# Optimization experiments

Hardware: AMD Instinct MI355X
Metric: run time of the kernel (lower is better)

## Reference

```python
import jax, jax.numpy as jnp
import numpy as np

EMB = 1024
NHEAD = 16
DILATIONS = (1, 4, 8, 16)
KSIZE = 7
ROT_DIM = 32  # RotaryEmbedding(dim=32): only first 32 channels of each head rotated


def neighbor_idx(T, k, d):
    # NATTEN-style 1D dilated neighborhood: window of k positions on the
    # dilation lattice (same residue class mod d), centered and clamped at borders.
    i = jnp.arange(T)
    r = i % d                      # residue class
    p = i // d                     # position within class
    Lr = (T - r + d - 1) // d      # class length
    s = jnp.clip(p - k // 2, 0, Lr - k)
    j = jnp.arange(k)
    return r[:, None] + (s[:, None] + j[None, :]) * d  # [T, k] int indices


def rope(x, rot_dim=ROT_DIM):
    # lucidrains RotaryEmbedding.rotate_queries_or_keys: interleaved pairs,
    # applied over seq dim (-2), only first rot_dim channels.
    T = x.shape[-2]
    inv = 1.0 / (10000.0 ** (jnp.arange(0, rot_dim, 2, dtype=jnp.float32) / rot_dim))
    freqs = jnp.arange(T, dtype=jnp.float32)[:, None] * inv[None, :]  # [T, rot_dim//2]
    freqs = jnp.repeat(freqs, 2, axis=-1)                             # [T, rot_dim]
    cos, sin = jnp.cos(freqs), jnp.sin(freqs)
    xr, xp = x[..., :rot_dim], x[..., rot_dim:]
    x1, x2 = xr[..., 0::2], xr[..., 1::2]
    rot = jnp.stack([-x2, x1], axis=-1).reshape(xr.shape)
    return jnp.concatenate([xr * cos + rot * sin, xp], axis=-1)


def setup_inputs() -> dict:
    key = jax.random.key(0)
    ks = jax.random.split(key, 5)
    B, T, C = 4, 8192, EMB
    s = 0.02
    return {
        "x": jax.random.normal(ks[0], (B, T, C), jnp.float32),
        "wq": jax.random.normal(ks[1], (C, C), jnp.float32) * s,
        "bq": jnp.zeros((C,), jnp.float32),
        "wk": jax.random.normal(ks[2], (C, C), jnp.float32) * s,
        "bk": jnp.zeros((C,), jnp.float32),
        "wv": jax.random.normal(ks[3], (C, C), jnp.float32) * s,
        "bv": jnp.zeros((C,), jnp.float32),
        "wp": jax.random.normal(ks[4], (C, C), jnp.float32) * s,
        "bp": jnp.zeros((C,), jnp.float32),
    }


def reference(x, wq, bq, wk, bk, wv, bv, wp, bp):
    B, T, C = x.shape
    hs = C // NHEAD

    def heads(w, b):  # torch Linear: x @ W^T + b, then [B, nh, T, hs]
        return (x @ w.T + b).reshape(B, T, NHEAD, hs).transpose(0, 2, 1, 3)

    q, k, v = heads(wq, bq), heads(wk, bk), heads(wv, bv)
    present = jnp.stack([k, v])  # pre-rotary kv cache, as in original

    q, k, v = rope(q), rope(k), rope(v)  # original also rotates v

    gsz = NHEAD // len(DILATIONS)
    outs = []
    for gi, d in enumerate(DILATIONS):
        sl = slice(gi * gsz, (gi + 1) * gsz)
        idx = neighbor_idx(T, KSIZE, d)           # [T, K]
        kk = k[:, sl][:, :, idx]                   # [B, g, T, K, hs]
        vv = v[:, sl][:, :, idx]                   # [B, g, T, K, hs]
        scores = jnp.einsum('bgtd,bgtkd->bgtk', q[:, sl], kk)  # no 1/sqrt(hs), as na1d_qk
        attn = jax.nn.softmax(scores, axis=-1)
        outs.append(jnp.einsum('bgtk,bgtkd->bgtd', attn, vv))
    y = jnp.concatenate(outs, axis=1)              # [B, nh, T, hs]
    y = y.transpose(0, 2, 1, 3).reshape(B, T, C)
    y = y @ wp.T + bp
    return (y, present)
```

## Files before the change

kernel.cpp:

```cpp
#include <hip/hip_runtime.h>

typedef unsigned short ushortT;
typedef unsigned int uint32;
typedef __attribute__((ext_vector_type(8))) short short8;
typedef __attribute__((ext_vector_type(4))) float f32x4;

__device__ __forceinline__ ushortT f2bf(float f) {
    uint32 u = __float_as_uint(f);
    uint32 r = (u + 0x7fffu + ((u >> 16) & 1u)) >> 16;
    return (ushortT)r;
}
__device__ __forceinline__ float bf2f(uint32 v) {
    return __uint_as_float(v << 16);
}

__device__ __forceinline__ void unpack8(uint4 v, float* f) {
    f[0] = bf2f(v.x & 0xffffu); f[1] = bf2f(v.x >> 16);
    f[2] = bf2f(v.y & 0xffffu); f[3] = bf2f(v.y >> 16);
    f[4] = bf2f(v.z & 0xffffu); f[5] = bf2f(v.z >> 16);
    f[6] = bf2f(v.w & 0xffffu); f[7] = bf2f(v.w >> 16);
}

typedef __attribute__((address_space(1))) const void gvoid;
typedef __attribute__((address_space(3))) void lvoid;
__device__ __forceinline__ void gld16(const ushortT* g, ushortT* l) {
    __builtin_amdgcn_global_load_lds((gvoid*)g, (lvoid*)l, 16, 0, 0);
}

__global__ __launch_bounds__(256) void f32_to_bf16_kernel(
    const float* __restrict__ src, ushortT* __restrict__ dst, int n4)
{
    int i = blockIdx.x * 256 + threadIdx.x;
    if (i < n4) {
        float4 v = reinterpret_cast<const float4*>(src)[i];
        ushort4 o;
        o.x = f2bf(v.x); o.y = f2bf(v.y); o.z = f2bf(v.z); o.w = f2bf(v.w);
        reinterpret_cast<ushort4*>(dst)[i] = o;
    }
}

__global__ __launch_bounds__(256) void rope_table_kernel(float2* __restrict__ tab)
{
    int idx = blockIdx.x * 256 + threadIdx.x;
    int t = idx >> 4;
    int i = idx & 15;
    float inv = powf(10000.0f, -(float)i / 16.0f);
    float ang = (float)t * inv;
    tab[idx] = make_float2(cosf(ang), sinf(ang));
}


__device__ __forceinline__ short8 ldsfrag(const ushortT* region, int row, int g) {
    int e = (row << 5) + (g << 3);
    e ^= ((row >> 1) & 3) << 3;
    return *reinterpret_cast<const short8*>(region + e);
}

template<int MODE>
__global__ __launch_bounds__(512, 2) void gemm256_kernel(
    const ushortT* __restrict__ A,
    const ushortT* __restrict__ W,
    const float*   __restrict__ bias,
    const float2*  __restrict__ tab,
    ushortT*       __restrict__ Cb,
    float*         __restrict__ Cf,
    int M, int N, int K)
{
    extern __shared__ ushortT lds[];
    const int tid  = threadIdx.x;
    const int lane = tid & 63;
    const int wv   = tid >> 6;
    const int wm   = wv >> 2;
    const int wn   = wv & 3;
    const int g    = lane >> 4;
    const int rsel = lane & 15;

    const int bid = blockIdx.x;
    const int swz = (bid & 7) * 64 + (bid >> 3);
    const int tm  = swz & 127, tn = swz >> 7;
    const int m0  = tm * 256,  n0 = tn * 256;

    const int crow = tid >> 2;
    const int ccol = ((tid & 3) ^ ((tid >> 3) & 3)) * 8;
    const ushortT* gA0 = A + (size_t)(m0 + crow) * K + ccol;
    const ushortT* gA1 = gA0 + (size_t)128 * K;
    const ushortT* gB0 = W + (size_t)(n0 + crow) * K + ccol;
    const ushortT* gB1 = gB0 + (size_t)128 * K;

    const int dst0 = wv * 512;
    const int dst1 = 4096 + wv * 512;

    #pragma unroll
    for (int t = 0; t < 3; ++t) {
        ushortT* ra = lds + t * 16384;
        ushortT* rb = ra + 8192;
        gld16(gA0 + t * 32, ra + dst0);
        gld16(gA1 + t * 32, ra + dst1);
        gld16(gB0 + t * 32, rb + dst0);
        gld16(gB1 + t * 32, rb + dst1);
    }
    asm volatile("s_waitcnt vmcnt(8)" ::: "memory");
    __builtin_amdgcn_s_barrier();

    f32x4 acc[8][4] = {};
    const int NT = K >> 5;

    #pragma unroll 1
    for (int t = 0; t < NT; ++t) {
        const ushortT* ra = lds + (t & 3) * 16384;
        const ushortT* rb = ra + 8192;

        short8 Bf[4], Af[4];
        #pragma unroll
        for (int fn = 0; fn < 4; ++fn) Bf[fn] = ldsfrag(rb, wn * 64 + fn * 16 + rsel, g);
        #pragma unroll
        for (int fm = 0; fm < 4; ++fm) Af[fm] = ldsfrag(ra, wm * 128 + fm * 16 + rsel, g);
        if (t + 3 < NT) {
            ushortT* wa = lds + ((t + 3) & 3) * 16384;
            gld16(gA0 + (t + 3) * 32, wa + dst0);
            gld16(gA1 + (t + 3) * 32, wa + dst1);
        }
        asm volatile("" ::: "memory");
        __builtin_amdgcn_s_barrier();
        asm volatile("s_waitcnt lgkmcnt(0)" ::: "memory");
        __builtin_amdgcn_sched_barrier(0);
        __builtin_amdgcn_s_setprio(1);
        #pragma unroll
        for (int fm = 0; fm < 4; ++fm)
            #pragma unroll
            for (int fn = 0; fn < 4; ++fn)
                acc[fm][fn] = __builtin_amdgcn_mfma_f32_16x16x32_bf16(Af[fm], Bf[fn], acc[fm][fn], 0, 0, 0);
        __builtin_amdgcn_s_setprio(0);
        asm volatile("" ::: "memory");
        __builtin_amdgcn_s_barrier();

        #pragma unroll
        for (int fm = 0; fm < 4; ++fm) Af[fm] = ldsfrag(ra, wm * 128 + 64 + fm * 16 + rsel, g);
        if (t + 3 < NT) {
            ushortT* wb = lds + ((t + 3) & 3) * 16384 + 8192;
            gld16(gB0 + (t + 3) * 32, wb + dst0);
            gld16(gB1 + (t + 3) * 32, wb + dst1);
        }
        if (t < NT - 3)      { asm volatile("s_waitcnt vmcnt(8)" ::: "memory"); }
        else if (t == NT - 3){ asm volatile("s_waitcnt vmcnt(4)" ::: "memory"); }
        else if (t == NT - 2){ asm volatile("s_waitcnt vmcnt(0)" ::: "memory"); }
        asm volatile("" ::: "memory");
        __builtin_amdgcn_s_barrier();
        asm volatile("s_waitcnt lgkmcnt(0)" ::: "memory");
        __builtin_amdgcn_sched_barrier(0);
        __builtin_amdgcn_s_setprio(1);
        #pragma unroll
        for (int fm = 0; fm < 4; ++fm)
            #pragma unroll
            for (int fn = 0; fn < 4; ++fn)
                acc[4 + fm][fn] = __builtin_amdgcn_mfma_f32_16x16x32_bf16(Af[fm], Bf[fn], acc[4 + fm][fn], 0, 0, 0);
        __builtin_amdgcn_s_setprio(0);
        asm volatile("" ::: "memory");
        __builtin_amdgcn_s_barrier();
    }

    #pragma unroll
    for (int fn = 0; fn < 4; ++fn) {
        const int colb = n0 + wn * 64 + fn * 16 + rsel;
        const int d    = colb & 63;
        const float bv = bias[colb];
        #pragma unroll
        for (int am = 0; am < 8; ++am) {
            const int rowbase = m0 + wm * 128 + am * 16 + g * 4;
            #pragma unroll
            for (int e = 0; e < 4; ++e) {
                const int row = rowbase + e;
                const float val = acc[am][fn][e] + bv;
                if (MODE == 1) {
                    const int b = row >> 13, t = row & 8191;
                    const int h = colb >> 6;
                    Cf[(((size_t)b * 16 + h) * 8192 + t) * 64 + d] = val;
                }
                if (MODE == 2) {
                    Cf[(size_t)row * N + colb] = val;
                } else {
                    const float pv = __shfl_xor(val, 1, 64);
                    float ov = val;
                    if (d < 32) {
                        const int t = row & 8191;
                        const float2 cs = tab[t * 16 + (d >> 1)];
                        ov = (d & 1) ? fmaf(val, cs.x,  pv * cs.y)
                                     : fmaf(val, cs.x, -pv * cs.y);
                    }
                    Cb[(size_t)row * N + colb] = f2bf(ov);
                }
            }
        }
    }
}

__global__ __launch_bounds__(256) void natt_kernel(
    const ushortT* __restrict__ Q,
    const ushortT* __restrict__ Kl,
    const ushortT* __restrict__ Vl,
    ushortT*       __restrict__ O)
{
    const int T = 8192;
    const int tid  = threadIdx.x;
    const int lane = tid & 63;
    const int tloc = lane >> 3;
    const int c    = lane & 7;

    const int wq   = (blockIdx.x * 256 + tid) >> 6;
    const int qidx = wq * 8 + tloc;
    const int t = qidx & (T - 1);
    const int h = (qidx >> 13) & 15;
    const int b = qidx >> 17;

    const int shifts[4] = {0, 2, 3, 4};
    const int sh = shifts[h >> 2];
    const int dd = 1 << sh;

    const int r  = t & (dd - 1);
    const int p  = t >> sh;
    const int Lr = ((T - 1 - r) >> sh) + 1;
    int s = p - 3;
    const int smax = Lr - 7;
    s = s < 0 ? 0 : (s > smax ? smax : s);
    const int tbase = r + (s << sh);

    const size_t qoff = ((size_t)(b * T + t)) * 1024 + h * 64 + c * 8;
    float qf[8];
    unpack8(*reinterpret_cast<const uint4*>(Q + qoff), qf);

    const size_t cbase = ((size_t)b * T) * 1024 + h * 64 + c * 8;

    float sc[7];
    #pragma unroll
    for (int j = 0; j < 7; ++j) {
        const int tj = tbase + (j << sh);
        float kf[8];
        unpack8(*reinterpret_cast<const uint4*>(Kl + cbase + (size_t)tj * 1024), kf);
        float pp = 0.f;
        #pragma unroll
        for (int i = 0; i < 8; ++i) pp = fmaf(qf[i], kf[i], pp);
        pp += __shfl_xor(pp, 1, 64);
        pp += __shfl_xor(pp, 2, 64);
        pp += __shfl_xor(pp, 4, 64);
        sc[j] = pp;
    }

    float mx = sc[0];
    #pragma unroll
    for (int j = 1; j < 7; ++j) mx = fmaxf(mx, sc[j]);
    float den = 0.f;
    #pragma unroll
    for (int j = 0; j < 7; ++j) { sc[j] = __expf(sc[j] - mx); den += sc[j]; }
    const float inv = 1.0f / den;

    float out[8] = {};
    #pragma unroll
    for (int j = 0; j < 7; ++j) {
        const int tj = tbase + (j << sh);
        float vf[8];
        unpack8(*reinterpret_cast<const uint4*>(Vl + cbase + (size_t)tj * 1024), vf);
        #pragma unroll
        for (int i = 0; i < 8; ++i) out[i] = fmaf(sc[j], vf[i], out[i]);
    }

    short8 ov;
    #pragma unroll
    for (int i = 0; i < 8; ++i) ov[i] = (short)f2bf(out[i] * inv);
    *reinterpret_cast<short8*>(const_cast<ushortT*>(O + qoff)) = ov;
}

extern "C" void kernel_launch(void* const* d_in, const int* in_sizes, int n_in,
                              void* d_out, int out_size, void* d_ws, size_t ws_size,
                              hipStream_t stream)
{
    const float* x  = (const float*)d_in[0];
    const float* wq = (const float*)d_in[1];
    const float* bq = (const float*)d_in[2];
    const float* wk = (const float*)d_in[3];
    const float* bk = (const float*)d_in[4];
    const float* wv = (const float*)d_in[5];
    const float* bv = (const float*)d_in[6];
    const float* wp = (const float*)d_in[7];
    const float* bp = (const float*)d_in[8];

    const int B = 4, T = 8192, C = 1024;
    const int M = B * T;
    const size_t MC = (size_t)M * C;

    char* ws = (char*)d_ws;
    ushortT* xb   = (ushortT*)ws;
    ushortT* wqb  = (ushortT*)(ws + (size_t)64 * 1024 * 1024);
    ushortT* wkb  = wqb + (size_t)C * C;
    ushortT* wvb  = wkb + (size_t)C * C;
    ushortT* wpb  = wvb + (size_t)C * C;
    ushortT* qlin = (ushortT*)(ws + (size_t)72 * 1024 * 1024);
    ushortT* klin = qlin + MC;
    ushortT* vlin = klin + MC;
    float2*  tab  = (float2*)(ws + (size_t)264 * 1024 * 1024);

    float* y     = (float*)d_out;
    float* presK = y + MC;
    float* presV = presK + MC;

    hipFuncSetAttribute((const void*)gemm256_kernel<0>,
                        hipFuncAttributeMaxDynamicSharedMemorySize, 131072);
    hipFuncSetAttribute((const void*)gemm256_kernel<1>,
                        hipFuncAttributeMaxDynamicSharedMemorySize, 131072);
    hipFuncSetAttribute((const void*)gemm256_kernel<2>,
                        hipFuncAttributeMaxDynamicSharedMemorySize, 131072);

    rope_table_kernel<<<512, 256, 0, stream>>>(tab);

    f32_to_bf16_kernel<<<(int)(MC / 4 / 256), 256, 0, stream>>>(x, xb, (int)(MC / 4));
    const int wn4 = C * C / 4;
    f32_to_bf16_kernel<<<(wn4 + 255) / 256, 256, 0, stream>>>(wq, wqb, wn4);
    f32_to_bf16_kernel<<<(wn4 + 255) / 256, 256, 0, stream>>>(wk, wkb, wn4);
    f32_to_bf16_kernel<<<(wn4 + 255) / 256, 256, 0, stream>>>(wv, wvb, wn4);
    f32_to_bf16_kernel<<<(wn4 + 255) / 256, 256, 0, stream>>>(wp, wpb, wn4);

    const int nwg = (M / 256) * (C / 256);
    gemm256_kernel<0><<<nwg, 512, 131072, stream>>>(xb, wqb, bq, tab, qlin, nullptr, M, C, C);
    gemm256_kernel<1><<<nwg, 512, 131072, stream>>>(xb, wkb, bk, tab, klin, presK, M, C, C);
    gemm256_kernel<1><<<nwg, 512, 131072, stream>>>(xb, wvb, bv, tab, vlin, presV, M, C, C);

    natt_kernel<<<(B * 16 * T) / 32, 256, 0, stream>>>(qlin, klin, vlin, xb);

    gemm256_kernel<2><<<nwg, 512, 131072, stream>>>(xb, wpb, bp, tab, nullptr, y, M, C, C);
}
```

Before: 623.0 us.

## Fuse Q, K and V projections into one N=3072 GEMM launch

Packs the Q, K and V weights and biases into contiguous buffers and runs a single GEMM over N=3072 instead of three separate GEMMs. The epilogue derives which projection a tile belongs to from its column, writes the rotated bf16 output at the matching offset and writes the fp32 present cache for K and V. The block swizzle is generalized to take the number of N tiles, so each group of row tiles reuses the same A tile across all 12 column tiles. This removes two launches and re-reads of x, at the cost of a bias packing kernel and slightly more index arithmetic in the epilogue.

```diff
diff --git a/kernel.cpp b/kernel.cpp
--- a/kernel.cpp
+++ b/kernel.cpp
@@ -39,6 +39,15 @@
     }
 }
 
+__global__ __launch_bounds__(256) void pack_bias_kernel(
+    const float* __restrict__ bq, const float* __restrict__ bk,
+    const float* __restrict__ bv, float* __restrict__ out)
+{
+    int i = blockIdx.x * 256 + threadIdx.x;
+    float v = (i < 1024) ? bq[i] : (i < 2048 ? bk[i - 1024] : bv[i - 2048]);
+    out[i] = v;
+}
+
 __global__ __launch_bounds__(256) void rope_table_kernel(float2* __restrict__ tab)
 {
     int idx = blockIdx.x * 256 + threadIdx.x;
@@ -56,7 +65,9 @@
     return *reinterpret_cast<const short8*>(region + e);
 }
 
-template<int MODE>
+#define MC_ ((size_t)33554432)
+
+template<int MODE, int NTN>
 __global__ __launch_bounds__(512, 2) void gemm256_kernel(
     const ushortT* __restrict__ A,
     const ushortT* __restrict__ W,
@@ -76,9 +87,11 @@
     const int rsel = lane & 15;
 
     const int bid = blockIdx.x;
-    const int swz = (bid & 7) * 64 + (bid >> 3);
-    const int tm  = swz & 127, tn = swz >> 7;
-    const int m0  = tm * 256,  n0 = tn * 256;
+    const int xi  = bid & 7;
+    const int j   = bid >> 3;
+    const int tn  = j % NTN;
+    const int tm  = xi * 16 + j / NTN;
+    const int m0  = tm * 256, n0 = tn * 256;
 
     const int crow = tid >> 2;
     const int ccol = ((tid & 3) ^ ((tid >> 3) & 3)) * 8;
@@ -159,9 +172,11 @@
         __builtin_amdgcn_s_barrier();
     }
 
+    const int proj = n0 >> 10;
     #pragma unroll
     for (int fn = 0; fn < 4; ++fn) {
         const int colb = n0 + wn * 64 + fn * 16 + rsel;
+        const int dcol = colb & 1023;
         const int d    = colb & 63;
         const float bv = bias[colb];
         #pragma unroll
@@ -171,14 +186,15 @@
             for (int e = 0; e < 4; ++e) {
                 const int row = rowbase + e;
                 const float val = acc[am][fn][e] + bv;
-                if (MODE == 1) {
-                    const int b = row >> 13, t = row & 8191;
-                    const int h = colb >> 6;
-                    Cf[(((size_t)b * 16 + h) * 8192 + t) * 64 + d] = val;
-                }
                 if (MODE == 2) {
                     Cf[(size_t)row * N + colb] = val;
                 } else {
+                    if (proj != 0) {
+                        const int b = row >> 13, t = row & 8191;
+                        const int h = dcol >> 6;
+                        Cf[(size_t)(proj - 1) * MC_ +
+                           (((size_t)b * 16 + h) * 8192 + t) * 64 + d] = val;
+                    }
                     const float pv = __shfl_xor(val, 1, 64);
                     float ov = val;
                     if (d < 32) {
@@ -187,7 +203,7 @@
                         ov = (d & 1) ? fmaf(val, cs.x,  pv * cs.y)
                                      : fmaf(val, cs.x, -pv * cs.y);
                     }
-                    Cb[(size_t)row * N + colb] = f2bf(ov);
+                    Cb[(size_t)proj * MC_ + (size_t)row * 1024 + dcol] = f2bf(ov);
                 }
             }
         }
@@ -288,42 +304,38 @@
     const size_t MC = (size_t)M * C;
 
     char* ws = (char*)d_ws;
-    ushortT* xb   = (ushortT*)ws;
-    ushortT* wqb  = (ushortT*)(ws + (size_t)64 * 1024 * 1024);
-    ushortT* wkb  = wqb + (size_t)C * C;
-    ushortT* wvb  = wkb + (size_t)C * C;
-    ushortT* wpb  = wvb + (size_t)C * C;
-    ushortT* qlin = (ushortT*)(ws + (size_t)72 * 1024 * 1024);
-    ushortT* klin = qlin + MC;
-    ushortT* vlin = klin + MC;
-    float2*  tab  = (float2*)(ws + (size_t)264 * 1024 * 1024);
+    ushortT* xb    = (ushortT*)ws;
+    ushortT* wqkvb = (ushortT*)(ws + (size_t)64 * 1024 * 1024);
+    ushortT* wpb   = wqkvb + (size_t)3 * C * C;
+    ushortT* qlin  = (ushortT*)(ws + (size_t)72 * 1024 * 1024);
+    ushortT* klin  = qlin + MC;
+    ushortT* vlin  = klin + MC;
+    float2*  tab   = (float2*)(ws + (size_t)264 * 1024 * 1024);
+    float*   bqkv  = (float*)(ws + (size_t)266 * 1024 * 1024);
 
     float* y     = (float*)d_out;
     float* presK = y + MC;
-    float* presV = presK + MC;
-
-    hipFuncSetAttribute((const void*)gemm256_kernel<0>,
+
+    hipFuncSetAttribute((const void*)gemm256_kernel<3, 12>,
                         hipFuncAttributeMaxDynamicSharedMemorySize, 131072);
-    hipFuncSetAttribute((const void*)gemm256_kernel<1>,
+    hipFuncSetAttribute((const void*)gemm256_kernel<2, 4>,
                         hipFuncAttributeMaxDynamicSharedMemorySize, 131072);
-    hipFuncSetAttribute((const void*)gemm256_kernel<2>,
-                        hipFuncAttributeMaxDynamicSharedMemorySize, 131072);
 
     rope_table_kernel<<<512, 256, 0, stream>>>(tab);
+    pack_bias_kernel<<<12, 256, 0, stream>>>(bq, bk, bv, bqkv);
 
     f32_to_bf16_kernel<<<(int)(MC / 4 / 256), 256, 0, stream>>>(x, xb, (int)(MC / 4));
     const int wn4 = C * C / 4;
-    f32_to_bf16_kernel<<<(wn4 + 255) / 256, 256, 0, stream>>>(wq, wqb, wn4);
-    f32_to_bf16_kernel<<<(wn4 + 255) / 256, 256, 0, stream>>>(wk, wkb, wn4);
-    f32_to_bf16_kernel<<<(wn4 + 255) / 256, 256, 0, stream>>>(wv, wvb, wn4);
+    f32_to_bf16_kernel<<<(wn4 + 255) / 256, 256, 0, stream>>>(wq, wqkvb, wn4);
+    f32_to_bf16_kernel<<<(wn4 + 255) / 256, 256, 0, stream>>>(wk, wqkvb + (size_t)C * C, wn4);
+    f32_to_bf16_kernel<<<(wn4 + 255) / 256, 256, 0, stream>>>(wv, wqkvb + (size_t)2 * C * C, wn4);
     f32_to_bf16_kernel<<<(wn4 + 255) / 256, 256, 0, stream>>>(wp, wpb, wn4);
 
-    const int nwg = (M / 256) * (C / 256);
-    gemm256_kernel<0><<<nwg, 512, 131072, stream>>>(xb, wqb, bq, tab, qlin, nullptr, M, C, C);
-    gemm256_kernel<1><<<nwg, 512, 131072, stream>>>(xb, wkb, bk, tab, klin, presK, M, C, C);
-    gemm256_kernel<1><<<nwg, 512, 131072, stream>>>(xb, wvb, bv, tab, vlin, presV, M, C, C);
+    gemm256_kernel<3, 12><<<1536, 512, 131072, stream>>>(
+        xb, wqkvb, bqkv, tab, qlin, presK, M, 3 * C, C);
 
     natt_kernel<<<(B * 16 * T) / 32, 256, 0, stream>>>(qlin, klin, vlin, xb);
 
-    gemm256_kernel<2><<<nwg, 512, 131072, stream>>>(xb, wpb, bp, tab, nullptr, y, M, C, C);
-}
+    gemm256_kernel<2, 4><<<512, 512, 131072, stream>>>(
+        xb, wpb, bp, tab, nullptr, y, M, C, C);
+}
```

Measured after the change: 651.2 us. +4.5%, slower.
